# Performance work log

Hardware: AMD Instinct MI355X
Metric: run time of the kernel (lower is better)

The kernel has to match this reference:

```python
import jax, jax.numpy as jnp
import numpy as np


def _lstm_cell(x, h, c, Wih, Whh, bih, bhh):
    # torch.nn.LSTMCell: gates ordered (input, forget, cell, output)
    g = x @ Wih.T + h @ Whh.T + bih + bhh
    i, f, gg, o = jnp.split(g, 4, axis=-1)
    c2 = jax.nn.sigmoid(f) * c + jax.nn.sigmoid(i) * jnp.tanh(gg)
    h2 = jax.nn.sigmoid(o) * jnp.tanh(c2)
    return h2, c2


def setup_inputs() -> dict:
    key = jax.random.key(0)
    T, B, S, D = 64, 16, 128, 512
    ks = jax.random.split(key, 10)
    sc = 0.04  # ~ 1/sqrt(D) init scale
    z2 = jnp.zeros((B, D), jnp.float32)
    return {
        "emb_utts": jax.random.normal(ks[0], (T, B, D), jnp.float32),
        "M": jax.random.normal(ks[1], (B, S, D), jnp.float32),
        "hr0": z2, "cr0": z2, "hw0": z2, "cw0": z2,
        "Wih_r": jax.random.normal(ks[2], (4 * D, D), jnp.float32) * sc,
        "Whh_r": jax.random.normal(ks[3], (4 * D, D), jnp.float32) * sc,
        "bih_r": jnp.zeros((4 * D,), jnp.float32),
        "bhh_r": jnp.zeros((4 * D,), jnp.float32),
        "Wih_w": jax.random.normal(ks[4], (4 * D, D), jnp.float32) * sc,
        "Whh_w": jax.random.normal(ks[5], (4 * D, D), jnp.float32) * sc,
        "bih_w": jnp.zeros((4 * D,), jnp.float32),
        "bhh_w": jnp.zeros((4 * D,), jnp.float32),
        "Wc": jax.random.normal(ks[6], (D, 2 * D), jnp.float32) * sc,
        "bc": jnp.zeros((D,), jnp.float32),
    }


def reference(emb_utts, M, hr0, cr0, hw0, cw0,
              Wih_r, Whh_r, bih_r, bhh_r,
              Wih_w, Whh_w, bih_w, bhh_w, Wc, bc):
    def step(carry, w):
        hr, cr, hw, cw, Mc = carry
        # read LSTM (dropout is identity in eval)
        hr, cr = _lstm_cell(w, hr, cr, Wih_r, Whh_r, bih_r, bhh_r)
        # attention over memory
        sim = jnp.einsum('bd,bsd->bs', hr, Mc)
        z = jax.nn.softmax(sim, axis=-1)
        m = jnp.einsum('bs,bsd->bd', z, Mc)
        # compose + write LSTM
        comp = jnp.concatenate([hr, m], axis=-1) @ Wc.T + bc
        hw, cw = _lstm_cell(comp, hw, cw, Wih_w, Whh_w, bih_w, bhh_w)
        # memory update, faithful to source: M_new = (1 - z) * (M + hw)
        erase = 1.0 - z[:, :, None]
        Mc = erase * (Mc + hw[:, None, :])
        return (hr, cr, hw, cw, Mc), hw

    (hr, cr, hw, cw, Mf), outputs = jax.lax.scan(
        step, (hr0, cr0, hw0, cw0, M), emb_utts)
    return outputs, hr, cr, hw, cw, Mf
```

## Files before the change

### kernel.cpp

```cpp
#include <hip/hip_runtime.h>
#include <math.h>

#define TT 64
#define BB 16
#define SS 128
#define DD 512
#define NBLK 256
#define NTH 256
#define BD (BB*DD)
#define OUT_HR   (TT*BD)
#define OUT_CR   (OUT_HR + BD)
#define OUT_HW   (OUT_CR + BD)
#define OUT_CW   (OUT_HW + BD)
#define OUT_MF   (OUT_CW + BD)
#define MAGIC 0x13579BDFu

#define SY_MASTER 64
#define SY_SHARD  256
#define SY_FLAG   2048

#define HRR_OFF 0
#define HWR_OFF 532480
#define MR_OFF  1064960
#define SP_OFF  1589248
#define GE_OFF  1622016

#define OFF_WHR  0
#define OFF_WHW  4672
#define OFF_WFH  9344
#define OFF_WFM  14016
#define OFF_ABUF 18688
#define OFF_ML   28160
#define OFF_PRED 32256
#define OFF_GFB  36480
#define OFF_GFT  36608
#define OFF_ZL   36736
#define OFF_BFL  36992
#define OFF_SMW  37000
#define LDS_FLOATS 37008
#define LDS_BYTES  (LDS_FLOATS*4)
#define KH_W 292
#define KH_A 592

#define COLC(c) (((c) >> 1) * DD + dr0 + ((c) & 1))

__device__ __forceinline__ float sigf(float x) { return 1.f / (1.f + __expf(-x)); }

__device__ __forceinline__ void stg(float* p, float v) {
  __hip_atomic_store(p, v, __ATOMIC_RELAXED, __HIP_MEMORY_SCOPE_AGENT);
}
__device__ __forceinline__ float ldga(const float* p) {
  return __hip_atomic_load(p, __ATOMIC_RELAXED, __HIP_MEMORY_SCOPE_AGENT);
}

__device__ __forceinline__ void barrive(unsigned* sync, unsigned& ep, int shard) {
  __syncthreads();
  if (threadIdx.x == 0) {
    ++ep;
    asm volatile("s_waitcnt vmcnt(0)" ::: "memory");
    unsigned o = __hip_atomic_fetch_add(sync + SY_SHARD + shard * 32, 1u,
                                        __ATOMIC_RELAXED, __HIP_MEMORY_SCOPE_AGENT);
    if ((o & 7u) == 7u) {
      unsigned m = __hip_atomic_fetch_add(sync + SY_MASTER, 1u,
                                          __ATOMIC_RELAXED, __HIP_MEMORY_SCOPE_AGENT);
      if (((m + 1u) & 31u) == 0u) {
        const unsigned done = (m + 1u) >> 5;
#pragma unroll
        for (int f = 0; f < 16; ++f)
          __hip_atomic_store(sync + SY_FLAG + f * 32, done,
                             __ATOMIC_RELAXED, __HIP_MEMORY_SCOPE_AGENT);
      }
    }
  }
}
__device__ __forceinline__ void bwait(unsigned* sync, unsigned ep, int fl) {
  if (threadIdx.x == 0) {
    const unsigned* p = sync + SY_FLAG + fl * 32;
    while (__hip_atomic_load(p, __ATOMIC_RELAXED, __HIP_MEMORY_SCOPE_AGENT) < ep) {
      __builtin_amdgcn_s_sleep(2);
    }
  }
  __syncthreads();
}
__device__ __forceinline__ void lbar(unsigned* sync, unsigned& ep, int shard, int fl) {
  barrive(sync, ep, shard);
  bwait(sync, ep, fl);
}

__device__ __forceinline__ float dotf4(const float* __restrict__ a,
                                       const float* __restrict__ b, int n4) {
  const float4* a4 = (const float4*)a;
  const float4* b4 = (const float4*)b;
  float4 s = make_float4(0.f, 0.f, 0.f, 0.f);
#pragma unroll 8
  for (int k = 0; k < n4; ++k) {
    float4 x = a4[k], y = b4[k];
    s.x = fmaf(x.x, y.x, s.x); s.y = fmaf(x.y, y.y, s.y);
    s.z = fmaf(x.z, y.z, s.z); s.w = fmaf(x.w, y.w, s.w);
  }
  return (s.x + s.y) + (s.z + s.w);
}

__device__ __forceinline__ void dot_pass8(const float* __restrict__ A,
                                          const float* __restrict__ W,
                                          float* __restrict__ pout)
{
  float acc[8] = {0.f,0.f,0.f,0.f,0.f,0.f,0.f,0.f};
#pragma unroll
  for (int j = 0; j < 8; ++j) {
    float4 a4 = *(const float4*)(A + j*4);
#pragma unroll
    for (int c = 0; c < 8; ++c) {
      float4 w4 = *(const float4*)(W + c*36 + j*4);
      acc[c] = fmaf(a4.x, w4.x, acc[c]); acc[c] = fmaf(a4.y, w4.y, acc[c]);
      acc[c] = fmaf(a4.z, w4.z, acc[c]); acc[c] = fmaf(a4.w, w4.w, acc[c]);
    }
  }
  *(float4*)(pout)   = make_float4(acc[0],acc[1],acc[2],acc[3]);
  *(float4*)(pout+4) = make_float4(acc[4],acc[5],acc[6],acc[7]);
}

__device__ __forceinline__ void dot_pass8g(const float* __restrict__ ag,
                                           const float* __restrict__ Wb,
                                           int khq,
                                           float* __restrict__ pout)
{
  float acc[8] = {0.f,0.f,0.f,0.f,0.f,0.f,0.f,0.f};
#pragma unroll
  for (int jj = 0; jj < 2; ++jj) {
    const float* Wt = Wb + (khq*2 + jj)*KH_W;
#pragma unroll
    for (int j = 0; j < 8; ++j) {
      float4 a4 = *(const float4*)(ag + jj*32 + j*4);
#pragma unroll
      for (int c = 0; c < 8; ++c) {
        float4 w4 = *(const float4*)(Wt + c*36 + j*4);
        acc[c] = fmaf(a4.x, w4.x, acc[c]); acc[c] = fmaf(a4.y, w4.y, acc[c]);
        acc[c] = fmaf(a4.z, w4.z, acc[c]); acc[c] = fmaf(a4.w, w4.w, acc[c]);
      }
    }
  }
  *(float4*)(pout)   = make_float4(acc[0],acc[1],acc[2],acc[3]);
  *(float4*)(pout+4) = make_float4(acc[4],acc[5],acc[6],acc[7]);
}

__global__ void __launch_bounds__(NTH) memnet(
    const float* __restrict__ emb, const float* __restrict__ M_in,
    const float* __restrict__ hr0, const float* __restrict__ cr0,
    const float* __restrict__ hw0, const float* __restrict__ cw0,
    const float* __restrict__ Wih_r, const float* __restrict__ Whh_r,
    const float* __restrict__ bih_r, const float* __restrict__ bhh_r,
    const float* __restrict__ Wih_w, const float* __restrict__ Whh_w,
    const float* __restrict__ bih_w, const float* __restrict__ bhh_w,
    const float* __restrict__ Wc, const float* __restrict__ bc,
    float* __restrict__ out,
    unsigned* sync, float* __restrict__ wsf)
{
  extern __shared__ float L[];
  const int tid = threadIdx.x;
  const int bid = blockIdx.x;
  const int shard = bid & 31;
  const int fl = bid & 15;

  const int mb  = bid & 15;
  const int mdh = bid >> 4;
  const int dr0 = 2 * bid;

  float* hrr = wsf + HRR_OFF;
  float* hwr = wsf + HWR_OFF;
  float* mr  = wsf + MR_OFF;
  float* sp  = wsf + SP_OFF;
  float* gE  = wsf + GE_OFF + bid * (TT * 128);

  if (bid == 0) {
    if (tid == 0) {
      __hip_atomic_store(sync + SY_MASTER, 0u, __ATOMIC_RELAXED, __HIP_MEMORY_SCOPE_AGENT);
#pragma unroll
      for (int k = 0; k < 32; ++k)
        __hip_atomic_store(sync + SY_SHARD + k * 32, 0u, __ATOMIC_RELAXED, __HIP_MEMORY_SCOPE_AGENT);
#pragma unroll
      for (int f = 0; f < 16; ++f)
        __hip_atomic_store(sync + SY_FLAG + f * 32, 0u, __ATOMIC_RELAXED, __HIP_MEMORY_SCOPE_AGENT);
      asm volatile("s_waitcnt vmcnt(0)" ::: "memory");
      __hip_atomic_store(sync, MAGIC, __ATOMIC_RELAXED, __HIP_MEMORY_SCOPE_AGENT);
    }
  } else if (tid == 0) {
    while (__hip_atomic_load(sync, __ATOMIC_RELAXED, __HIP_MEMORY_SCOPE_AGENT) != MAGIC) {}
  }
  __syncthreads();
  unsigned ep = 0;

  float cr = 0.f, cw = 0.f;
  if (tid >= 128 && tid < 160) {
    const int t = tid - 128, b = t & 15, dl = t >> 4;
    cr = cr0[b * DD + dr0 + dl];
    cw = cw0[b * DD + dr0 + dl];
  }

  {
    float* wih = L + OFF_ABUF;
#pragma unroll
    for (int c = 0; c < 8; ++c)
      ((float2*)(wih + c * DD))[tid] = ((const float2*)(Wih_w + COLC(c) * DD))[tid];
  }
  __syncthreads();
  {
    const float* wih = L + OFF_ABUF;
    float4 acc[8];
#pragma unroll
    for (int c = 0; c < 8; ++c) acc[c] = make_float4(0.f,0.f,0.f,0.f);
    const int k0 = tid * 4;
    for (int cc = 0; cc < DD; ++cc) {
      float4 wc4 = *(const float4*)(Wc + cc * 1024 + k0);
#pragma unroll
      for (int c = 0; c < 8; ++c) {
        const float wv = wih[c * DD + cc];
        acc[c].x = fmaf(wv, wc4.x, acc[c].x); acc[c].y = fmaf(wv, wc4.y, acc[c].y);
        acc[c].z = fmaf(wv, wc4.z, acc[c].z); acc[c].w = fmaf(wv, wc4.w, acc[c].w);
      }
    }
    const int kk = k0 & 511, kh = kk >> 5, jf = kk & 31;
    float* Tb = L + ((k0 < 512) ? OFF_WFH : OFF_WFM);
#pragma unroll
    for (int c = 0; c < 8; ++c)
      *(float4*)(Tb + kh*KH_W + c*36 + jf) = acc[c];
    if (tid < 8) {
      float s = 0.f;
      for (int cc = 0; cc < DD; ++cc) s = fmaf(wih[tid * DD + cc], bc[cc], s);
      L[OFF_BFL + tid] = s + bih_w[COLC(tid)] + bhh_w[COLC(tid)];
    }
  }
  __syncthreads();
  {
    const int c = tid >> 5, r = tid & 31;
    const int kk = r * 16, kh = kk >> 5, jb = (r & 1) * 16;
#pragma unroll
    for (int set = 0; set < 2; ++set) {
      const float* Wsrc = set ? Whh_w : Whh_r;
      float* dst = L + (set ? OFF_WHW : OFF_WHR) + kh*KH_W + c*36 + jb;
      const float* src = Wsrc + COLC(c) * DD + kk;
#pragma unroll
      for (int u = 0; u < 4; ++u)
        *(float4*)(dst + u*4) = *(const float4*)(src + u*4);
    }
  }
  {
    const int d_l = tid >> 3, sq = tid & 7;
    const int d = mdh * 32 + d_l;
#pragma unroll 4
    for (int j = 0; j < 16; ++j) {
      const int s = sq * 16 + j;
      L[OFF_ML + d_l * 128 + s] = M_in[(mb * SS + s) * DD + d];
    }
  }
  {
    const int tH = tid >> 7, b = (tid >> 3) & 15, c = tid & 7;
    const int col = COLC(c);
    const float bias = bih_r[col] + bhh_r[col];
    const float* wrow = Wih_r + col * DD;
    for (int t = tH * 32; t < tH * 32 + 32; ++t) {
      gE[t * 128 + b * 8 + c] = dotf4(emb + (t * BB + b) * DD, wrow, DD / 4) + bias;
    }
  }
  __syncthreads();
  {
#pragma unroll
    for (int j = 0; j < 8; ++j) {
      const int idx = j * 256 + tid;
      const int b = idx >> 7, k4 = idx & 127;
      const int kh = k4 >> 3, jf = (k4 & 7) * 4;
      float4 v = ((const float4*)hr0)[idx];
      *(float4*)(L + OFF_ABUF + kh*KH_A + b*36 + jf) = v;
    }
  }
  __syncthreads();
  {
    const int kh = tid >> 4, b = tid & 15;
    dot_pass8(L + OFF_ABUF + kh*KH_A + b*36, L + OFF_WHR + kh*KH_W,
              L + OFF_PRED + kh*132 + b*8);
  }
  __syncthreads();
  if (tid < 128) {
    float s = 0.f;
#pragma unroll
    for (int k2 = 0; k2 < 16; ++k2) s += L[OFF_PRED + k2*132 + tid];
    L[OFF_GFT + tid] = s;
  }
  __syncthreads();
  if (tid >= 128 && tid < 160) {
    const int t = tid - 128, b = t & 15, dl = t >> 4;
    float g[4];
#pragma unroll
    for (int q = 0; q < 4; ++q) {
      const int bc = b * 8 + q * 2 + dl;
      g[q] = L[OFF_GFT + bc] + gE[0 * 128 + bc];
    }
    cr = sigf(g[1]) * cr + sigf(g[0]) * tanhf(g[2]);
    const float h2 = sigf(g[3]) * tanhf(cr);
    stg(hrr + 1 * BD + b * DD + dr0 + dl, h2);
  }
  lbar(sync, ep, shard, fl);
  {
    const float* src = hrr + 1 * BD;
#pragma unroll
    for (int j = 0; j < 8; ++j) {
      const int idx = j * 256 + tid;
      const int b = idx >> 7, k4 = idx & 127;
      const int kh = k4 >> 3, jf = (k4 & 7) * 4;
      float4 v = ((const float4*)src)[idx];
      *(float4*)(L + OFF_ABUF + kh*KH_A + b*36 + jf) = v;
    }
  }
  __syncthreads();

  for (int i = 0; i < TT; ++i) {
    const int ii = i + 1;
    float* zold = L + OFF_ZL + ((i & 1) ^ 1) * 128;
    float* znew = L + OFF_ZL + (i & 1) * 128;

    {
      const int d_l = tid >> 3, sq = tid & 7;
      const float* Mrow = L + OFF_ML + d_l * 128;
      const float hrv = L[OFF_ABUF + mdh*KH_A + mb*36 + d_l];
#pragma unroll
      for (int j = 0; j < 4; ++j) {
        const int s4 = sq * 16 + j * 4;
        float4 M4 = *(const float4*)(Mrow + s4);
        float4 s;
        s.x = hrv * M4.x; s.y = hrv * M4.y; s.z = hrv * M4.z; s.w = hrv * M4.w;
        *(float4*)(L + OFF_PRED + d_l*132 + s4) = s;
      }
    }
    __syncthreads();
    if (tid < SS) {
      float v = 0.f;
#pragma unroll
      for (int dl2 = 0; dl2 < 32; ++dl2) v += L[OFF_PRED + dl2*132 + tid];
      stg(sp + (mb * 16 + mdh) * SS + tid, v);
    }
    barrive(sync, ep, shard);

    if (ii < TT) {
      {
        const int kh = tid >> 4, b = tid & 15;
        dot_pass8(L + OFF_ABUF + kh*KH_A + b*36, L + OFF_WHR + kh*KH_W,
                  L + OFF_PRED + kh*132 + b*8);
      }
      __syncthreads();
      if (tid < 128) {
        float s = 0.f;
#pragma unroll
        for (int k2 = 0; k2 < 16; ++k2) s += L[OFF_PRED + k2*132 + tid];
        L[OFF_GFT + tid] = s;
      }
      __syncthreads();
      if (tid >= 128 && tid < 160) {
        const int t = tid - 128, b = t & 15, dl = t >> 4;
        float g[4];
#pragma unroll
        for (int q = 0; q < 4; ++q) {
          const int bc = b * 8 + q * 2 + dl;
          g[q] = L[OFF_GFT + bc] + gE[ii * 128 + bc];
        }
        cr = sigf(g[1]) * cr + sigf(g[0]) * tanhf(g[2]);
        const float h2 = sigf(g[3]) * tanhf(cr);
        stg(hrr + (ii + 1) * BD + b * DD + dr0 + dl, h2);
        if (ii == TT - 1) {
          out[OUT_HR + b * DD + dr0 + dl] = h2;
          out[OUT_CR + b * DD + dr0 + dl] = cr;
        }
      }
    }
    bwait(sync, ep, fl);

    float vsum = 0.f;
    if (tid < SS) {
#pragma unroll
      for (int j = 0; j < 16; ++j) vsum += ldga(sp + (mb * 16 + j) * SS + tid);
    } else if (i > 0) {
      const int t = tid - 128, k0 = t * 4;
      const float4 hw4 = *(const float4*)(hwr + i * BD + mb * DD + k0);
      const float4 a4  = *(const float4*)(L + OFF_ABUF + (k0 >> 5)*KH_A + mb*36 + (k0 & 31));
      float p = a4.x * hw4.x;
      p = fmaf(a4.y, hw4.y, p); p = fmaf(a4.z, hw4.z, p); p = fmaf(a4.w, hw4.w, p);
      for (int off = 32; off > 0; off >>= 1) p += __shfl_xor(p, off);
      if ((tid & 63) == 0) L[OFF_SMW + 6 + ((tid >> 6) & 1)] = p;
    }
    __syncthreads();
    if (tid < SS) {
      float v = vsum;
      if (i > 0) {
        const float hrdot = L[OFF_SMW + 6] + L[OFF_SMW + 7];
        v = (1.f - zold[tid]) * (v + hrdot);
      }
      float wm = v;
      for (int off = 32; off > 0; off >>= 1) wm = fmaxf(wm, __shfl_xor(wm, off));
      if ((tid & 63) == 0) L[OFF_SMW + (tid >> 6)] = wm;
      vsum = v;
    }
    __syncthreads();
    if (tid < SS) {
      const float gmax = fmaxf(L[OFF_SMW], L[OFF_SMW + 1]);
      const float e = __expf(vsum - gmax);
      float sm = e;
      for (int off = 32; off > 0; off >>= 1) sm += __shfl_xor(sm, off);
      if ((tid & 63) == 0) L[OFF_SMW + 2 + (tid >> 6)] = sm;
      vsum = e;
    }
    __syncthreads();
    if (tid < SS) znew[tid] = vsum / (L[OFF_SMW + 2] + L[OFF_SMW + 3]);
    __syncthreads();
    {
      const int d_l = tid >> 3, sq = tid & 7;
      float* Mrow = L + OFF_ML + d_l * 128;
      float mv = 0.f;
      if (i > 0) {
        const float hwv = hwr[i * BD + mb * DD + mdh * 32 + d_l];
#pragma unroll
        for (int j = 0; j < 4; ++j) {
          const int s4 = sq * 16 + j * 4;
          float4 M4  = *(float4*)(Mrow + s4);
          float4 zo4 = *(const float4*)(zold + s4);
          float4 zn4 = *(const float4*)(znew + s4);
          M4.x = (1.f - zo4.x) * (M4.x + hwv);
          M4.y = (1.f - zo4.y) * (M4.y + hwv);
          M4.z = (1.f - zo4.z) * (M4.z + hwv);
          M4.w = (1.f - zo4.w) * (M4.w + hwv);
          *(float4*)(Mrow + s4) = M4;
          mv = fmaf(zn4.x, M4.x, mv); mv = fmaf(zn4.y, M4.y, mv);
          mv = fmaf(zn4.z, M4.z, mv); mv = fmaf(zn4.w, M4.w, mv);
        }
      } else {
#pragma unroll
        for (int j = 0; j < 4; ++j) {
          const int s4 = sq * 16 + j * 4;
          float4 M4  = *(const float4*)(Mrow + s4);
          float4 zn4 = *(const float4*)(znew + s4);
          mv = fmaf(zn4.x, M4.x, mv); mv = fmaf(zn4.y, M4.y, mv);
          mv = fmaf(zn4.z, M4.z, mv); mv = fmaf(zn4.w, M4.w, mv);
        }
      }
      L[OFF_PRED + d_l * 8 + sq] = mv;
    }
    __syncthreads();
    if (tid < 32) {
      float mv = 0.f;
#pragma unroll
      for (int j = 0; j < 8; ++j) mv += L[OFF_PRED + tid * 8 + j];
      stg(mr + i * BD + mb * DD + mdh * 32 + tid, mv);
    }
    barrive(sync, ep, shard);

    {
      const int kh = tid >> 4, b = tid & 15;
      dot_pass8(L + OFF_ABUF + kh*KH_A + b*36, L + OFF_WFH + kh*KH_W,
                L + OFF_PRED + 2112 + kh*132 + b*8);
    }
    __syncthreads();
    if (tid < 128) {
      float s = 0.f;
#pragma unroll
      for (int k2 = 0; k2 < 16; ++k2) s += L[OFF_PRED + 2112 + k2*132 + tid];
      L[OFF_GFB + tid] = s;
    }
    bwait(sync, ep, fl);

    {
      const int src = tid >> 7, khq = (tid >> 4) & 7, b = tid & 15;
      const float* ag;
      const float* Wb;
      if (src == 0) { ag = mr + i * BD + b * DD + khq * 64; Wb = L + OFF_WFM; }
      else {
        const float* hwsrc = (i == 0) ? hw0 : (hwr + i * BD);
        ag = hwsrc + b * DD + khq * 64; Wb = L + OFF_WHW;
      }
      dot_pass8g(ag, Wb, khq, L + OFF_PRED + (src * 8 + khq) * 132 + b * 8);
    }
    __syncthreads();
    if (tid < 128) {
      float s = 0.f;
#pragma unroll
      for (int k2 = 0; k2 < 16; ++k2) s += L[OFF_PRED + k2*132 + tid];
      L[OFF_GFT + tid] = s;
    }
    __syncthreads();
    if (tid >= 128 && tid < 160) {
      const int t = tid - 128, b = t & 15, dl = t >> 4;
      float g[4];
#pragma unroll
      for (int q = 0; q < 4; ++q) {
        const int c = q * 2 + dl, bc = b * 8 + c;
        g[q] = L[OFF_GFB + bc] + L[OFF_GFT + bc] + L[OFF_BFL + c];
      }
      cw = sigf(g[1]) * cw + sigf(g[0]) * tanhf(g[2]);
      const float h2 = sigf(g[3]) * tanhf(cw);
      const int d = dr0 + dl;
      stg(hwr + (i + 1) * BD + b * DD + d, h2);
      out[i * BD + b * DD + d] = h2;
      if (i == TT - 1) {
        out[OUT_HW + b * DD + d] = h2;
        out[OUT_CW + b * DD + d] = cw;
      }
    }
    if (i < TT - 1) {
      const float* src = hrr + (i + 2) * BD;
#pragma unroll
      for (int j = 0; j < 8; ++j) {
        const int idx = j * 256 + tid;
        const int b = idx >> 7, k4 = idx & 127;
        const int kh = k4 >> 3, jf = (k4 & 7) * 4;
        float4 v = ((const float4*)src)[idx];
        *(float4*)(L + OFF_ABUF + kh*KH_A + b*36 + jf) = v;
      }
    }
    __syncthreads();
  }

  lbar(sync, ep, shard, fl);

  {
    const int d_l = tid >> 3, sq = tid & 7;
    const int d = mdh * 32 + d_l;
    const float hwv = hwr[TT * BD + mb * DD + d];
    const float* zfin = L + OFF_ZL + ((TT - 1) & 1) * 128;
#pragma unroll 4
    for (int j = 0; j < 16; ++j) {
      const int s = sq * 16 + j;
      const float nv = (1.f - zfin[s]) * (L[OFF_ML + d_l * 128 + s] + hwv);
      out[OUT_MF + (mb * SS + s) * DD + d] = nv;
    }
  }
}

extern "C" void kernel_launch(void* const* d_in, const int* in_sizes, int n_in,
                              void* d_out, int out_size, void* d_ws, size_t ws_size,
                              hipStream_t stream) {
  (void)in_sizes; (void)n_in; (void)out_size; (void)ws_size;
  const float* emb   = (const float*)d_in[0];
  const float* M_in  = (const float*)d_in[1];
  const float* hr0   = (const float*)d_in[2];
  const float* cr0   = (const float*)d_in[3];
  const float* hw0   = (const float*)d_in[4];
  const float* cw0   = (const float*)d_in[5];
  const float* Wih_r = (const float*)d_in[6];
  const float* Whh_r = (const float*)d_in[7];
  const float* bih_r = (const float*)d_in[8];
  const float* bhh_r = (const float*)d_in[9];
  const float* Wih_w = (const float*)d_in[10];
  const float* Whh_w = (const float*)d_in[11];
  const float* bih_w = (const float*)d_in[12];
  const float* bhh_w = (const float*)d_in[13];
  const float* Wc    = (const float*)d_in[14];
  const float* bc    = (const float*)d_in[15];
  float* out = (float*)d_out;

  char* wsb = (char*)d_ws;
  unsigned* sync = (unsigned*)wsb;
  float* wsf = (float*)(wsb + 16384);

  hipFuncSetAttribute((const void*)memnet,
                      hipFuncAttributeMaxDynamicSharedMemorySize, LDS_BYTES);

  hipLaunchKernelGGL(memnet, dim3(NBLK), dim3(NTH), LDS_BYTES, stream,
                     emb, M_in, hr0, cr0, hw0, cw0,
                     Wih_r, Whh_r, bih_r, bhh_r,
                     Wih_w, Whh_w, bih_w, bhh_w, Wc, bc,
                     out, sync, wsf);
}
```

Baseline: 1.565 ms.

## Replace global grid barrier with row/column group barriers for attention phase

The hierarchical shard/master/flag grid barrier becomes a flat 8-counter sum barrier, and the mid-step global barrier around the similarity partials is replaced by smaller barriers over the 16 blocks of a row or column. The hr·hw correction term is now computed as distributed per-block partials exchanged through global memory. The memory update is moved ahead of the column wait so it overlaps the synchronization. This is meant to cut grid-wide sync latency per timestep, at the cost of extra atomics and an additional exchange round trip.

```diff
diff --git a/kernel.cpp b/kernel.cpp
--- a/kernel.cpp
+++ b/kernel.cpp
@@ -15,9 +15,10 @@
 #define OUT_MF   (OUT_CW + BD)
 #define MAGIC 0x13579BDFu
 
-#define SY_MASTER 64
-#define SY_SHARD  256
-#define SY_FLAG   2048
+#define SY_GSH  256
+#define SY_COL  1024
+#define SY_ROW  1536
+#define SY_PC   3072
 
 #define HRR_OFF 0
 #define HWR_OFF 532480
@@ -37,7 +38,8 @@
 #define OFF_ZL   36736
 #define OFF_BFL  36992
 #define OFF_SMW  37000
-#define LDS_FLOATS 37008
+#define OFF_PCL  37008
+#define LDS_FLOATS 37024
 #define LDS_BYTES  (LDS_FLOATS*4)
 #define KH_W 292
 #define KH_A 592
@@ -53,38 +55,33 @@
   return __hip_atomic_load(p, __ATOMIC_RELAXED, __HIP_MEMORY_SCOPE_AGENT);
 }
 
-__device__ __forceinline__ void barrive(unsigned* sync, unsigned& ep, int shard) {
+__device__ __forceinline__ void g_arrive(unsigned* sync, unsigned& gep, int shard) {
   __syncthreads();
   if (threadIdx.x == 0) {
-    ++ep;
+    ++gep;
     asm volatile("s_waitcnt vmcnt(0)" ::: "memory");
-    unsigned o = __hip_atomic_fetch_add(sync + SY_SHARD + shard * 32, 1u,
-                                        __ATOMIC_RELAXED, __HIP_MEMORY_SCOPE_AGENT);
-    if ((o & 7u) == 7u) {
-      unsigned m = __hip_atomic_fetch_add(sync + SY_MASTER, 1u,
-                                          __ATOMIC_RELAXED, __HIP_MEMORY_SCOPE_AGENT);
-      if (((m + 1u) & 31u) == 0u) {
-        const unsigned done = (m + 1u) >> 5;
-#pragma unroll
-        for (int f = 0; f < 16; ++f)
-          __hip_atomic_store(sync + SY_FLAG + f * 32, done,
-                             __ATOMIC_RELAXED, __HIP_MEMORY_SCOPE_AGENT);
-      }
-    }
-  }
-}
-__device__ __forceinline__ void bwait(unsigned* sync, unsigned ep, int fl) {
+    __hip_atomic_fetch_add(sync + SY_GSH + shard * 64, 1u,
+                           __ATOMIC_RELAXED, __HIP_MEMORY_SCOPE_AGENT);
+  }
+}
+__device__ __forceinline__ void g_wait(unsigned* sync, unsigned gep) {
   if (threadIdx.x == 0) {
-    const unsigned* p = sync + SY_FLAG + fl * 32;
-    while (__hip_atomic_load(p, __ATOMIC_RELAXED, __HIP_MEMORY_SCOPE_AGENT) < ep) {
-      __builtin_amdgcn_s_sleep(2);
-    }
-  }
-  __syncthreads();
-}
-__device__ __forceinline__ void lbar(unsigned* sync, unsigned& ep, int shard, int fl) {
-  barrive(sync, ep, shard);
-  bwait(sync, ep, fl);
+    const unsigned target = gep * (unsigned)NBLK;
+    for (;;) {
+      unsigned s = 0;
+#pragma unroll
+      for (int k = 0; k < 8; ++k)
+        s += __hip_atomic_load(sync + SY_GSH + k * 64,
+                               __ATOMIC_RELAXED, __HIP_MEMORY_SCOPE_AGENT);
+      if (s >= target) break;
+      __builtin_amdgcn_s_sleep(1);
+    }
+  }
+  __syncthreads();
+}
+__device__ __forceinline__ void g_bar(unsigned* sync, unsigned& gep, int shard) {
+  g_arrive(sync, gep, shard);
+  g_wait(sync, gep);
 }
 
 __device__ __forceinline__ float dotf4(const float* __restrict__ a,
@@ -159,12 +156,15 @@
   extern __shared__ float L[];
   const int tid = threadIdx.x;
   const int bid = blockIdx.x;
-  const int shard = bid & 31;
-  const int fl = bid & 15;
+  const int gsh = bid & 7;
 
   const int mb  = bid & 15;
   const int mdh = bid >> 4;
   const int dr0 = 2 * bid;
+
+  unsigned* colp = sync + SY_COL + mb  * 32;
+  unsigned* rowp = sync + SY_ROW + mdh * 32;
+  float*    pcp  = (float*)(sync + SY_PC);
 
   float* hrr = wsf + HRR_OFF;
   float* hwr = wsf + HWR_OFF;
@@ -174,13 +174,14 @@
 
   if (bid == 0) {
     if (tid == 0) {
-      __hip_atomic_store(sync + SY_MASTER, 0u, __ATOMIC_RELAXED, __HIP_MEMORY_SCOPE_AGENT);
-#pragma unroll
-      for (int k = 0; k < 32; ++k)
-        __hip_atomic_store(sync + SY_SHARD + k * 32, 0u, __ATOMIC_RELAXED, __HIP_MEMORY_SCOPE_AGENT);
-#pragma unroll
-      for (int f = 0; f < 16; ++f)
-        __hip_atomic_store(sync + SY_FLAG + f * 32, 0u, __ATOMIC_RELAXED, __HIP_MEMORY_SCOPE_AGENT);
+#pragma unroll
+      for (int k = 0; k < 8; ++k)
+        __hip_atomic_store(sync + SY_GSH + k * 64, 0u, __ATOMIC_RELAXED, __HIP_MEMORY_SCOPE_AGENT);
+#pragma unroll
+      for (int k = 0; k < 16; ++k) {
+        __hip_atomic_store(sync + SY_COL + k * 32, 0u, __ATOMIC_RELAXED, __HIP_MEMORY_SCOPE_AGENT);
+        __hip_atomic_store(sync + SY_ROW + k * 32, 0u, __ATOMIC_RELAXED, __HIP_MEMORY_SCOPE_AGENT);
+      }
       asm volatile("s_waitcnt vmcnt(0)" ::: "memory");
       __hip_atomic_store(sync, MAGIC, __ATOMIC_RELAXED, __HIP_MEMORY_SCOPE_AGENT);
     }
@@ -188,7 +189,7 @@
     while (__hip_atomic_load(sync, __ATOMIC_RELAXED, __HIP_MEMORY_SCOPE_AGENT) != MAGIC) {}
   }
   __syncthreads();
-  unsigned ep = 0;
+  unsigned gep = 0;
 
   float cr = 0.f, cw = 0.f;
   if (tid >= 128 && tid < 160) {
@@ -299,7 +300,7 @@
     const float h2 = sigf(g[3]) * tanhf(cr);
     stg(hrr + 1 * BD + b * DD + dr0 + dl, h2);
   }
-  lbar(sync, ep, shard, fl);
+  g_bar(sync, gep, gsh);
   {
     const float* src = hrr + 1 * BD;
 #pragma unroll
@@ -317,6 +318,7 @@
     const int ii = i + 1;
     float* zold = L + OFF_ZL + ((i & 1) ^ 1) * 128;
     float* znew = L + OFF_ZL + (i & 1) * 128;
+    const unsigned grp_tgt = 16u * (unsigned)(i + 1);
 
     {
       const int d_l = tid >> 3, sq = tid & 7;
@@ -338,7 +340,11 @@
       for (int dl2 = 0; dl2 < 32; ++dl2) v += L[OFF_PRED + dl2*132 + tid];
       stg(sp + (mb * 16 + mdh) * SS + tid, v);
     }
-    barrive(sync, ep, shard);
+    __syncthreads();
+    if (tid == 0) {
+      asm volatile("s_waitcnt vmcnt(0)" ::: "memory");
+      __hip_atomic_fetch_add(rowp, 1u, __ATOMIC_RELAXED, __HIP_MEMORY_SCOPE_AGENT);
+    }
 
     if (ii < TT) {
       {
@@ -371,27 +377,60 @@
         }
       }
     }
-    bwait(sync, ep, fl);
+    if (tid == 0) {
+      while (__hip_atomic_load(rowp, __ATOMIC_RELAXED, __HIP_MEMORY_SCOPE_AGENT) < grp_tgt) {}
+    }
+    __syncthreads();
+
+    if (i > 0 && tid < 32) {
+      float p = L[OFF_ABUF + mdh*KH_A + mb*36 + tid] *
+                hwr[i * BD + mb * DD + mdh * 32 + tid];
+      p += __shfl_xor(p, 16); p += __shfl_xor(p, 8); p += __shfl_xor(p, 4);
+      p += __shfl_xor(p, 2);  p += __shfl_xor(p, 1);
+      if (tid == 0) stg(pcp + mb * 16 + mdh, p);
+    }
+    __syncthreads();
+    if (tid == 0) {
+      asm volatile("s_waitcnt vmcnt(0)" ::: "memory");
+      __hip_atomic_fetch_add(colp, 1u, __ATOMIC_RELAXED, __HIP_MEMORY_SCOPE_AGENT);
+    }
+
+    if (i > 0) {
+      const int d_l = tid >> 3, sq = tid & 7;
+      float* Mrow = L + OFF_ML + d_l * 128;
+      const float hwv = hwr[i * BD + mb * DD + mdh * 32 + d_l];
+#pragma unroll
+      for (int j = 0; j < 4; ++j) {
+        const int s4 = sq * 16 + j * 4;
+        float4 M4  = *(float4*)(Mrow + s4);
+        float4 zo4 = *(const float4*)(zold + s4);
+        M4.x = (1.f - zo4.x) * (M4.x + hwv);
+        M4.y = (1.f - zo4.y) * (M4.y + hwv);
+        M4.z = (1.f - zo4.z) * (M4.z + hwv);
+        M4.w = (1.f - zo4.w) * (M4.w + hwv);
+        *(float4*)(Mrow + s4) = M4;
+      }
+    }
+    if (tid == 0) {
+      while (__hip_atomic_load(colp, __ATOMIC_RELAXED, __HIP_MEMORY_SCOPE_AGENT) < grp_tgt) {}
+    }
+    __syncthreads();
 
     float vsum = 0.f;
     if (tid < SS) {
 #pragma unroll
       for (int j = 0; j < 16; ++j) vsum += ldga(sp + (mb * 16 + j) * SS + tid);
-    } else if (i > 0) {
-      const int t = tid - 128, k0 = t * 4;
-      const float4 hw4 = *(const float4*)(hwr + i * BD + mb * DD + k0);
-      const float4 a4  = *(const float4*)(L + OFF_ABUF + (k0 >> 5)*KH_A + mb*36 + (k0 & 31));
-      float p = a4.x * hw4.x;
-      p = fmaf(a4.y, hw4.y, p); p = fmaf(a4.z, hw4.z, p); p = fmaf(a4.w, hw4.w, p);
-      for (int off = 32; off > 0; off >>= 1) p += __shfl_xor(p, off);
-      if ((tid & 63) == 0) L[OFF_SMW + 6 + ((tid >> 6) & 1)] = p;
+    } else if (i > 0 && tid >= 128 && tid < 144) {
+      L[OFF_PCL + (tid - 128)] = ldga(pcp + mb * 16 + (tid - 128));
     }
     __syncthreads();
     if (tid < SS) {
       float v = vsum;
       if (i > 0) {
-        const float hrdot = L[OFF_SMW + 6] + L[OFF_SMW + 7];
-        v = (1.f - zold[tid]) * (v + hrdot);
+        float c = 0.f;
+#pragma unroll
+        for (int k = 0; k < 16; ++k) c += L[OFF_PCL + k];
+        v = (1.f - zold[tid]) * (v + c);
       }
       float wm = v;
       for (int off = 32; off > 0; off >>= 1) wm = fmaxf(wm, __shfl_xor(wm, off));
@@ -410,35 +449,18 @@
     __syncthreads();
     if (tid < SS) znew[tid] = vsum / (L[OFF_SMW + 2] + L[OFF_SMW + 3]);
     __syncthreads();
+
     {
       const int d_l = tid >> 3, sq = tid & 7;
-      float* Mrow = L + OFF_ML + d_l * 128;
+      const float* Mrow = L + OFF_ML + d_l * 128;
       float mv = 0.f;
-      if (i > 0) {
-        const float hwv = hwr[i * BD + mb * DD + mdh * 32 + d_l];
-#pragma unroll
-        for (int j = 0; j < 4; ++j) {
-          const int s4 = sq * 16 + j * 4;
-          float4 M4  = *(float4*)(Mrow + s4);
-          float4 zo4 = *(const float4*)(zold + s4);
-          float4 zn4 = *(const float4*)(znew + s4);
-          M4.x = (1.f - zo4.x) * (M4.x + hwv);
-          M4.y = (1.f - zo4.y) * (M4.y + hwv);
-          M4.z = (1.f - zo4.z) * (M4.z + hwv);
-          M4.w = (1.f - zo4.w) * (M4.w + hwv);
-          *(float4*)(Mrow + s4) = M4;
-          mv = fmaf(zn4.x, M4.x, mv); mv = fmaf(zn4.y, M4.y, mv);
-          mv = fmaf(zn4.z, M4.z, mv); mv = fmaf(zn4.w, M4.w, mv);
-        }
-      } else {
-#pragma unroll
-        for (int j = 0; j < 4; ++j) {
-          const int s4 = sq * 16 + j * 4;
-          float4 M4  = *(const float4*)(Mrow + s4);
-          float4 zn4 = *(const float4*)(znew + s4);
-          mv = fmaf(zn4.x, M4.x, mv); mv = fmaf(zn4.y, M4.y, mv);
-          mv = fmaf(zn4.z, M4.z, mv); mv = fmaf(zn4.w, M4.w, mv);
-        }
+#pragma unroll
+      for (int j = 0; j < 4; ++j) {
+        const int s4 = sq * 16 + j * 4;
+        float4 z4 = *(const float4*)(znew + s4);
+        float4 M4 = *(const float4*)(Mrow + s4);
+        mv = fmaf(z4.x, M4.x, mv); mv = fmaf(z4.y, M4.y, mv);
+        mv = fmaf(z4.z, M4.z, mv); mv = fmaf(z4.w, M4.w, mv);
       }
       L[OFF_PRED + d_l * 8 + sq] = mv;
     }
@@ -449,7 +471,7 @@
       for (int j = 0; j < 8; ++j) mv += L[OFF_PRED + tid * 8 + j];
       stg(mr + i * BD + mb * DD + mdh * 32 + tid, mv);
     }
-    barrive(sync, ep, shard);
+    g_arrive(sync, gep, gsh);
 
     {
       const int kh = tid >> 4, b = tid & 15;
@@ -463,7 +485,7 @@
       for (int k2 = 0; k2 < 16; ++k2) s += L[OFF_PRED + 2112 + k2*132 + tid];
       L[OFF_GFB + tid] = s;
     }
-    bwait(sync, ep, fl);
+    g_wait(sync, gep);
 
     {
       const int src = tid >> 7, khq = (tid >> 4) & 7, b = tid & 15;
@@ -516,7 +538,7 @@
     __syncthreads();
   }
 
-  lbar(sync, ep, shard, fl);
+  g_bar(sync, gep, gsh);
 
   {
     const int d_l = tid >> 3, sq = tid & 7;
```

After: 1.504 ms. 3.9% less time.

## Replace hierarchical atomic grid barrier with per-block epoch flags polled by all threads

Applied to the files above, without the earlier changes.

The two-level grid barrier (shard counters feeding a master counter that then broadcasts 16 flags) is replaced by a flat scheme. Each block publishes its epoch to its own padded slot, and every thread of every block polls one of the 256 slots until all have reached the epoch. This removes the serialized atomic fetch-add chain and the flag broadcast from the barrier's critical path. In exchange, all 256 blocks now poll global memory each barrier, which adds polling traffic, and the sleep interval is shorter.

```diff
diff --git a/kernel.cpp b/kernel.cpp
--- a/kernel.cpp
+++ b/kernel.cpp
@@ -15,9 +15,7 @@
 #define OUT_MF   (OUT_CW + BD)
 #define MAGIC 0x13579BDFu
 
-#define SY_MASTER 64
-#define SY_SHARD  256
-#define SY_FLAG   2048
+#define SY_SLOT 256
 
 #define HRR_OFF 0
 #define HWR_OFF 532480
@@ -53,38 +51,25 @@
   return __hip_atomic_load(p, __ATOMIC_RELAXED, __HIP_MEMORY_SCOPE_AGENT);
 }
 
-__device__ __forceinline__ void barrive(unsigned* sync, unsigned& ep, int shard) {
-  __syncthreads();
+__device__ __forceinline__ void barrive(unsigned* sync, unsigned& ep) {
+  __syncthreads();
+  ++ep;
   if (threadIdx.x == 0) {
-    ++ep;
     asm volatile("s_waitcnt vmcnt(0)" ::: "memory");
-    unsigned o = __hip_atomic_fetch_add(sync + SY_SHARD + shard * 32, 1u,
-                                        __ATOMIC_RELAXED, __HIP_MEMORY_SCOPE_AGENT);
-    if ((o & 7u) == 7u) {
-      unsigned m = __hip_atomic_fetch_add(sync + SY_MASTER, 1u,
-                                          __ATOMIC_RELAXED, __HIP_MEMORY_SCOPE_AGENT);
-      if (((m + 1u) & 31u) == 0u) {
-        const unsigned done = (m + 1u) >> 5;
-#pragma unroll
-        for (int f = 0; f < 16; ++f)
-          __hip_atomic_store(sync + SY_FLAG + f * 32, done,
-                             __ATOMIC_RELAXED, __HIP_MEMORY_SCOPE_AGENT);
-      }
-    }
-  }
-}
-__device__ __forceinline__ void bwait(unsigned* sync, unsigned ep, int fl) {
-  if (threadIdx.x == 0) {
-    const unsigned* p = sync + SY_FLAG + fl * 32;
-    while (__hip_atomic_load(p, __ATOMIC_RELAXED, __HIP_MEMORY_SCOPE_AGENT) < ep) {
-      __builtin_amdgcn_s_sleep(2);
-    }
-  }
-  __syncthreads();
-}
-__device__ __forceinline__ void lbar(unsigned* sync, unsigned& ep, int shard, int fl) {
-  barrive(sync, ep, shard);
-  bwait(sync, ep, fl);
+    __hip_atomic_store(sync + SY_SLOT + blockIdx.x * 8, ep,
+                       __ATOMIC_RELAXED, __HIP_MEMORY_SCOPE_AGENT);
+  }
+}
+__device__ __forceinline__ void bwait(unsigned* sync, unsigned ep) {
+  const unsigned* slot = sync + SY_SLOT + threadIdx.x * 8;
+  while (__hip_atomic_load(slot, __ATOMIC_RELAXED, __HIP_MEMORY_SCOPE_AGENT) < ep) {
+    __builtin_amdgcn_s_sleep(1);
+  }
+  __syncthreads();
+}
+__device__ __forceinline__ void lbar(unsigned* sync, unsigned& ep) {
+  barrive(sync, ep);
+  bwait(sync, ep);
 }
 
 __device__ __forceinline__ float dotf4(const float* __restrict__ a,
@@ -159,8 +144,6 @@
   extern __shared__ float L[];
   const int tid = threadIdx.x;
   const int bid = blockIdx.x;
-  const int shard = bid & 31;
-  const int fl = bid & 15;
 
   const int mb  = bid & 15;
   const int mdh = bid >> 4;
@@ -173,14 +156,10 @@
   float* gE  = wsf + GE_OFF + bid * (TT * 128);
 
   if (bid == 0) {
+    __hip_atomic_store(sync + SY_SLOT + tid * 8, 0u,
+                       __ATOMIC_RELAXED, __HIP_MEMORY_SCOPE_AGENT);
+    __syncthreads();
     if (tid == 0) {
-      __hip_atomic_store(sync + SY_MASTER, 0u, __ATOMIC_RELAXED, __HIP_MEMORY_SCOPE_AGENT);
-#pragma unroll
-      for (int k = 0; k < 32; ++k)
-        __hip_atomic_store(sync + SY_SHARD + k * 32, 0u, __ATOMIC_RELAXED, __HIP_MEMORY_SCOPE_AGENT);
-#pragma unroll
-      for (int f = 0; f < 16; ++f)
-        __hip_atomic_store(sync + SY_FLAG + f * 32, 0u, __ATOMIC_RELAXED, __HIP_MEMORY_SCOPE_AGENT);
       asm volatile("s_waitcnt vmcnt(0)" ::: "memory");
       __hip_atomic_store(sync, MAGIC, __ATOMIC_RELAXED, __HIP_MEMORY_SCOPE_AGENT);
     }
@@ -299,7 +278,7 @@
     const float h2 = sigf(g[3]) * tanhf(cr);
     stg(hrr + 1 * BD + b * DD + dr0 + dl, h2);
   }
-  lbar(sync, ep, shard, fl);
+  lbar(sync, ep);
   {
     const float* src = hrr + 1 * BD;
 #pragma unroll
@@ -338,7 +317,7 @@
       for (int dl2 = 0; dl2 < 32; ++dl2) v += L[OFF_PRED + dl2*132 + tid];
       stg(sp + (mb * 16 + mdh) * SS + tid, v);
     }
-    barrive(sync, ep, shard);
+    barrive(sync, ep);
 
     if (ii < TT) {
       {
@@ -371,7 +350,7 @@
         }
       }
     }
-    bwait(sync, ep, fl);
+    bwait(sync, ep);
 
     float vsum = 0.f;
     if (tid < SS) {
@@ -449,7 +428,7 @@
       for (int j = 0; j < 8; ++j) mv += L[OFF_PRED + tid * 8 + j];
       stg(mr + i * BD + mb * DD + mdh * 32 + tid, mv);
     }
-    barrive(sync, ep, shard);
+    barrive(sync, ep);
 
     {
       const int kh = tid >> 4, b = tid & 15;
@@ -463,7 +442,7 @@
       for (int k2 = 0; k2 < 16; ++k2) s += L[OFF_PRED + 2112 + k2*132 + tid];
       L[OFF_GFB + tid] = s;
     }
-    bwait(sync, ep, fl);
+    bwait(sync, ep);
 
     {
       const int src = tid >> 7, khq = (tid >> 4) & 7, b = tid & 15;
@@ -516,7 +495,7 @@
     __syncthreads();
   }
 
-  lbar(sync, ep, shard, fl);
+  lbar(sync, ep);
 
   {
     const int d_l = tid >> 3, sq = tid & 7;
```

Result: faster. 1.463 ms (-6.5%).
